# Performance work log

Hardware: AMD Instinct MI355X
Metric: run time of the kernel (lower is better)

The kernel has to match this reference:

```python
import jax, jax.numpy as jnp
import numpy as np

B, S, HID = 4, 2048, 1024
H, D = 16, 64  # num_attention_heads, attention_head_size


def setup_inputs() -> dict:
    key = jax.random.key(0)
    k1, k2, k3, k4 = jax.random.split(key, 4)
    scale = 0.02
    return {
        "hidden_states": jax.random.normal(k1, (B, S, HID), dtype=jnp.float32),
        "attention_mask": jnp.zeros((B, 1, 1, S), dtype=jnp.float32),
        "Wq": jax.random.normal(k2, (HID, HID), dtype=jnp.float32) * scale,
        "bq": jnp.zeros((HID,), dtype=jnp.float32),
        "Wk": jax.random.normal(k3, (HID, HID), dtype=jnp.float32) * scale,
        "bk": jnp.zeros((HID,), dtype=jnp.float32),
        "Wv": jax.random.normal(k4, (HID, HID), dtype=jnp.float32) * scale,
        "bv": jnp.zeros((HID,), dtype=jnp.float32),
    }


def _split_heads(x):
    # [B,S,HID] -> [B,H,S,D]
    b, s, _ = x.shape
    return x.reshape(b, s, H, D).transpose(0, 2, 1, 3)


def reference(hidden_states, attention_mask, Wq, bq, Wk, bk, Wv, bv):
    # nn.Linear applies x @ W.T + b
    q = _split_heads(hidden_states @ Wq.T + bq)  # [B,H,S,D]
    k = _split_heads(hidden_states @ Wk.T + bk)
    v = _split_heads(hidden_states @ Wv.T + bv)
    scores = jnp.einsum("bhqd,bhkd->bhqk", q, k) / jnp.sqrt(jnp.float32(D))
    scores = scores + attention_mask  # additive mask, broadcast [B,1,1,S]
    probs = jax.nn.softmax(scores, axis=-1)  # dropout prob = 0 -> identity
    ctx = jnp.einsum("bhqk,bhkd->bhqd", probs, v)  # [B,H,S,D]
    ctx = ctx.transpose(0, 2, 1, 3).reshape(hidden_states.shape[0], hidden_states.shape[1], HID)
    return ctx
```

## Files before the change

### kernel.cpp

```cpp
#include <hip/hip_runtime.h>
#include <stdint.h>

#define BB 4
#define SS 2048
#define HID 1024
#define NH 16
#define DH 64

using bf16x8 = __attribute__((ext_vector_type(8))) short;
using f32x4  = __attribute__((ext_vector_type(4))) float;

#define LOG2E 1.44269504088896340736f

__device__ __forceinline__ ushort f2bf(float f) {
  union { float f; uint32_t u; } v; v.f = f;
  return (ushort)((v.u + 0x7FFFu + ((v.u >> 16) & 1u)) >> 16);
}

__device__ __forceinline__ uint32_t cvt_pk_bf16(float a, float b) {
  uint32_t r;
  asm("v_cvt_pk_bf16_f32 %0, %1, %2" : "=v"(r) : "v"(a), "v"(b));
  return r;
}

__device__ __forceinline__ float exp2_hw(float x) {
  float r;
  asm("v_exp_f32 %0, %1" : "=v"(r) : "v"(x));
  return r;
}

__device__ __forceinline__ void gload_lds16(const ushort* g, ushort* l) {
  __builtin_amdgcn_global_load_lds(
      (const __attribute__((address_space(1))) uint32_t*)g,
      (__attribute__((address_space(3))) uint32_t*)l, 16, 0, 0);
}

__device__ __forceinline__ int vperm(int j) {
  return (j & 0x23) | ((j & 0x0C) << 1) | ((j & 0x10) >> 2);
}

__global__ void cvt_kernel(const float* __restrict__ x, const float* __restrict__ wq,
                           const float* __restrict__ wk, const float* __restrict__ wv,
                           const float* __restrict__ am,
                           ushort* __restrict__ xbf, ushort* __restrict__ wbf,
                           float* __restrict__ maskL) {
  const int64_t NX4 = (int64_t)BB * SS * HID / 4;
  const int64_t NW4 = (int64_t)HID * HID / 4;
  const int64_t NWT = 3 * NW4;
  int64_t i = (int64_t)blockIdx.x * blockDim.x + threadIdx.x;
  if (i >= NX4 + NWT) {
    const int64_t jm = i - (NX4 + NWT);
    float4 v = ((const float4*)am)[jm];
    v.x *= LOG2E; v.y *= LOG2E; v.z *= LOG2E; v.w *= LOG2E;
    ((float4*)maskL)[jm] = v;
    return;
  }
  float4 v;
  ushort4* dst;
  if (i < NX4) {
    v = ((const float4*)x)[i];
    dst = (ushort4*)xbf + i;
  } else {
    int64_t j = i - NX4;
    int w = (int)(j >> 18);
    int64_t k = j & (NW4 - 1);
    const float* src = (w == 0) ? wq : (w == 1) ? wk : wv;
    v = ((const float4*)src)[k];
    dst = (ushort4*)wbf + j;
  }
  ushort4 o;
  o.x = f2bf(v.x); o.y = f2bf(v.y); o.z = f2bf(v.z); o.w = f2bf(v.w);
  *dst = o;
}

__global__ __launch_bounds__(256) void qkv_gemm(
    const ushort* __restrict__ xbf, const ushort* __restrict__ wbf,
    const float* __restrict__ bq, const float* __restrict__ bk,
    const float* __restrict__ bv,
    ushort* __restrict__ qws, ushort* __restrict__ kws, ushort* __restrict__ vtws) {
  __shared__ short Al[2][128][32];
  __shared__ short Bl[2][128][32];
  const int tid = threadIdx.x, wid = tid >> 6, lane = tid & 63;
  const int m0 = blockIdx.x * 128, n0 = blockIdx.y * 128;
  const int wr = wid >> 1, wc = wid & 1;

  f32x4 acc[4][4];
#pragma unroll
  for (int i = 0; i < 4; ++i)
#pragma unroll
    for (int j = 0; j < 4; ++j)
#pragma unroll
      for (int r = 0; r < 4; ++r) acc[i][j][r] = 0.f;

  const int srow = wid * 32 + (lane >> 2);
  const int scol = (lane & 3) * 8;
  const ushort* ga = xbf + (int64_t)(m0 + srow) * HID + scol;
  const ushort* gb = wbf + (int64_t)(n0 + srow) * HID + scol;

  auto stage = [&](int bufsel, int kb) {
    const ushort* a = ga + kb * 32;
    const ushort* b = gb + kb * 32;
    gload_lds16(a,            (ushort*)&Al[bufsel][wid * 32][0]);
    gload_lds16(a + 16 * HID, (ushort*)&Al[bufsel][wid * 32 + 16][0]);
    gload_lds16(b,            (ushort*)&Bl[bufsel][wid * 32][0]);
    gload_lds16(b + 16 * HID, (ushort*)&Bl[bufsel][wid * 32 + 16][0]);
  };

  stage(0, 0);
  __syncthreads();
  const int colL = lane & 15, rowg = lane >> 4;
  for (int kb = 0; kb < HID / 32; ++kb) {
    const int buf = kb & 1;
    if (kb + 1 < HID / 32) stage(buf ^ 1, kb + 1);
    bf16x8 af[4], bfr[4];
#pragma unroll
    for (int i = 0; i < 4; ++i)
      af[i] = *(const bf16x8*)&Al[buf][wr * 64 + i * 16 + colL][rowg * 8];
#pragma unroll
    for (int j = 0; j < 4; ++j)
      bfr[j] = *(const bf16x8*)&Bl[buf][wc * 64 + j * 16 + colL][rowg * 8];
#pragma unroll
    for (int i = 0; i < 4; ++i)
#pragma unroll
      for (int j = 0; j < 4; ++j)
        acc[i][j] = __builtin_amdgcn_mfma_f32_16x16x32_bf16(af[i], bfr[j], acc[i][j], 0, 0, 0);
    __syncthreads();
  }

#pragma unroll
  for (int j = 0; j < 4; ++j) {
    const int n = n0 + wc * 64 + j * 16 + colL;
    const int which = n >> 10;
    const int c = n & 1023;
    const int h = c >> 6, d = c & 63;
    const float bias = ((which == 0) ? bq : (which == 1) ? bk : bv)[c];
#pragma unroll
    for (int i = 0; i < 4; ++i) {
      const int mb = m0 + wr * 64 + i * 16 + rowg * 4;
      const int b = mb >> 11, s = mb & 2047;
      const int bh = b * NH + h;
      if (which == 2) {
        ushort4 o;
        o.x = f2bf(acc[i][j][0] + bias);
        o.y = f2bf(acc[i][j][1] + bias);
        o.z = f2bf(acc[i][j][2] + bias);
        o.w = f2bf(acc[i][j][3] + bias);
        const int scol2 = (s & ~63) | vperm(s & 63);
        *(ushort4*)&vtws[((int64_t)bh * DH + d) * SS + scol2] = o;
      } else {
        ushort* dst = (which == 0) ? qws : kws;
#pragma unroll
        for (int r = 0; r < 4; ++r)
          dst[((int64_t)bh * SS + s + r) * DH + d] = f2bf(acc[i][j][r] + bias);
      }
    }
  }
}

__global__ __launch_bounds__(256, 4) void attn_kernel(
    const ushort* __restrict__ qws, const ushort* __restrict__ kws,
    const ushort* __restrict__ vtws, const float* __restrict__ maskL,
    float* __restrict__ out) {
  __shared__ short Kl[2][64][64];
  __shared__ short Vl[2][64][64];

  const int tid = threadIdx.x, wid = tid >> 6, lane = tid & 63;
  const int bh = blockIdx.x, qb = blockIdx.y;
  const int b = bh >> 4, h = bh & 15;
  const int64_t qkb = (int64_t)bh * SS * DH;
  const int64_t vb  = (int64_t)bh * DH * SS;
  const int q0 = qb * 128;
  const int colL = lane & 15, rowg = lane >> 4;
  const float SCL = 0.125f * LOG2E;

  const int srow = wid * 16 + (lane >> 3);
  const int swzc = (((lane & 7) * 16) ^ ((lane >> 3) << 4)) >> 1;
  const ushort* gk = kws + qkb + (int64_t)srow * DH + swzc;
  const ushort* gv = vtws + vb + (int64_t)srow * SS + swzc;
  ushort* ldsK = (ushort*)&Kl[0][0][0] + wid * 1024;
  ushort* ldsV = (ushort*)&Vl[0][0][0] + wid * 1024;

  auto stageKV = [&](int bufsel, int tt) {
    const ushort* k0 = gk + tt * 4096;
    gload_lds16(k0,       ldsK + bufsel * 4096);
    gload_lds16(k0 + 512, ldsK + bufsel * 4096 + 512);
    const ushort* v0 = gv + tt * 64;
    gload_lds16(v0,          ldsV + bufsel * 4096);
    gload_lds16(v0 + 8 * SS, ldsV + bufsel * 4096 + 512);
  };

  const int xsw = (colL & 7) << 4;
  const char* kb0 = (const char*)&Kl[0][0][0] + colL * 128 + ((rowg * 16) ^ xsw);
  const char* kb1 = (const char*)&Kl[0][0][0] + colL * 128 + ((64 + rowg * 16) ^ xsw);
  const char* vb0 = (const char*)&Vl[0][0][0] + colL * 128 + ((rowg * 16) ^ xsw);
  const char* vb1 = (const char*)&Vl[0][0][0] + colL * 128 + ((64 + rowg * 16) ^ xsw);

  bf16x8 qf[2][2];
#pragma unroll
  for (int qh = 0; qh < 2; ++qh) {
    const ushort* gq = qws + qkb + (int64_t)(q0 + wid * 32 + qh * 16 + colL) * DH + rowg * 8;
    qf[qh][0] = *(const bf16x8*)(gq);
    qf[qh][1] = *(const bf16x8*)(gq + 32);
  }

  const f32x4 FZERO = {0.f, 0.f, 0.f, 0.f};
  union OU { uint32_t u[4]; bf16x8 v; } onesu;
  onesu.u[0] = 0x3F803F80u; onesu.u[1] = 0x3F803F80u;
  onesu.u[2] = 0x3F803F80u; onesu.u[3] = 0x3F803F80u;
  const bf16x8 ONES = onesu.v;

  f32x4 accO[2][4];
  f32x4 accL[2];
#pragma unroll
  for (int qh = 0; qh < 2; ++qh) {
    accL[qh] = FZERO;
#pragma unroll
    for (int dt = 0; dt < 4; ++dt)
#pragma unroll
      for (int r = 0; r < 4; ++r) accO[qh][dt][r] = 0.f;
  }

  const float* mrow = maskL + b * SS + rowg * 4;

  stageKV(0, 0);
  __syncthreads();

  auto step = [&](int t, int bufc) {
    if (t + 1 < SS / 64) stageKV(bufc ^ 1, t + 1);

    f32x4 sc[2][4];
    __builtin_amdgcn_s_setprio(1);
#pragma unroll
    for (int kt = 0; kt < 4; ++kt) {
      bf16x8 kf0 = *(const bf16x8*)(kb0 + bufc * 8192 + kt * 2048);
      bf16x8 kf1 = *(const bf16x8*)(kb1 + bufc * 8192 + kt * 2048);
      sc[0][kt] = __builtin_amdgcn_mfma_f32_16x16x32_bf16(kf0, qf[0][0], FZERO, 0, 0, 0);
      sc[0][kt] = __builtin_amdgcn_mfma_f32_16x16x32_bf16(kf1, qf[0][1], sc[0][kt], 0, 0, 0);
      sc[1][kt] = __builtin_amdgcn_mfma_f32_16x16x32_bf16(kf0, qf[1][0], FZERO, 0, 0, 0);
      sc[1][kt] = __builtin_amdgcn_mfma_f32_16x16x32_bf16(kf1, qf[1][1], sc[1][kt], 0, 0, 0);
    }
    __builtin_amdgcn_s_setprio(0);

    float4 m4[4];
#pragma unroll
    for (int kt = 0; kt < 4; ++kt)
      m4[kt] = *(const float4*)(mrow + t * 64 + kt * 16);

    bf16x8 paf[2][2];
#pragma unroll
    for (int qh = 0; qh < 2; ++qh) {
#pragma unroll
      for (int kt = 0; kt < 4; ++kt) {
        sc[qh][kt][0] = exp2_hw(fmaf(sc[qh][kt][0], SCL, m4[kt].x));
        sc[qh][kt][1] = exp2_hw(fmaf(sc[qh][kt][1], SCL, m4[kt].y));
        sc[qh][kt][2] = exp2_hw(fmaf(sc[qh][kt][2], SCL, m4[kt].z));
        sc[qh][kt][3] = exp2_hw(fmaf(sc[qh][kt][3], SCL, m4[kt].w));
      }
      union PU { uint32_t u[4]; bf16x8 v; } p0, p1;
      p0.u[0] = cvt_pk_bf16(sc[qh][0][0], sc[qh][0][1]);
      p0.u[1] = cvt_pk_bf16(sc[qh][0][2], sc[qh][0][3]);
      p0.u[2] = cvt_pk_bf16(sc[qh][1][0], sc[qh][1][1]);
      p0.u[3] = cvt_pk_bf16(sc[qh][1][2], sc[qh][1][3]);
      p1.u[0] = cvt_pk_bf16(sc[qh][2][0], sc[qh][2][1]);
      p1.u[1] = cvt_pk_bf16(sc[qh][2][2], sc[qh][2][3]);
      p1.u[2] = cvt_pk_bf16(sc[qh][3][0], sc[qh][3][1]);
      p1.u[3] = cvt_pk_bf16(sc[qh][3][2], sc[qh][3][3]);
      paf[qh][0] = p0.v;
      paf[qh][1] = p1.v;
    }

    __builtin_amdgcn_s_setprio(1);
#pragma unroll
    for (int ks = 0; ks < 2; ++ks) {
      accL[0] = __builtin_amdgcn_mfma_f32_16x16x32_bf16(paf[0][ks], ONES, accL[0], 0, 0, 0);
      accL[1] = __builtin_amdgcn_mfma_f32_16x16x32_bf16(paf[1][ks], ONES, accL[1], 0, 0, 0);
#pragma unroll
      for (int dt = 0; dt < 4; ++dt) {
        bf16x8 vf = *(const bf16x8*)((ks == 0 ? vb0 : vb1) + bufc * 8192 + dt * 2048);
        accO[0][dt] = __builtin_amdgcn_mfma_f32_16x16x32_bf16(paf[0][ks], vf, accO[0][dt], 0, 0, 0);
        accO[1][dt] = __builtin_amdgcn_mfma_f32_16x16x32_bf16(paf[1][ks], vf, accO[1][dt], 0, 0, 0);
      }
    }
    __builtin_amdgcn_s_setprio(0);
    __syncthreads();
  };

  for (int t = 0; t < SS / 64; t += 2) {
    step(t, 0);
    step(t + 1, 1);
  }

#pragma unroll
  for (int qh = 0; qh < 2; ++qh) {
    float inv[4];
#pragma unroll
    for (int r = 0; r < 4; ++r) inv[r] = 1.0f / accL[qh][r];
#pragma unroll
    for (int dt = 0; dt < 4; ++dt)
#pragma unroll
      for (int r = 0; r < 4; ++r) {
        const int s = q0 + wid * 32 + qh * 16 + rowg * 4 + r;
        out[((int64_t)b * SS + s) * HID + h * DH + dt * 16 + colL] = accO[qh][dt][r] * inv[r];
      }
  }
}

extern "C" void kernel_launch(void* const* d_in, const int* in_sizes, int n_in,
                              void* d_out, int out_size, void* d_ws, size_t ws_size,
                              hipStream_t stream) {
  const float* x  = (const float*)d_in[0];
  const float* am = (const float*)d_in[1];
  const float* wq = (const float*)d_in[2];
  const float* bq = (const float*)d_in[3];
  const float* wk = (const float*)d_in[4];
  const float* bk = (const float*)d_in[5];
  const float* wv = (const float*)d_in[6];
  const float* bv = (const float*)d_in[7];
  float* out = (float*)d_out;
  char* ws = (char*)d_ws;

  ushort* xbf  = (ushort*)(ws);
  ushort* wbf  = (ushort*)(ws + 16777216);
  ushort* qws  = (ushort*)(ws + 23068672);
  ushort* kws  = (ushort*)(ws + 39845888);
  ushort* vtws = (ushort*)(ws + 56623104);
  float*  mskL = (float*)(ws + 73400320);

  hipLaunchKernelGGL(cvt_kernel, dim3(11272), dim3(256), 0, stream,
                     x, wq, wk, wv, am, xbf, wbf, mskL);
  hipLaunchKernelGGL(qkv_gemm, dim3(64, 24), dim3(256), 0, stream,
                     xbf, wbf, bq, bk, bv, qws, kws, vtws);
  hipLaunchKernelGGL(attn_kernel, dim3(64, 16), dim3(256), 0, stream,
                     qws, kws, vtws, mskL, out);
}
```

Before: 168.2 us.

## Rewrite QKV GEMM with 256x256 tiles, swizzled LDS, and phased prefetch pipeline

```diff
diff --git a/kernel.cpp b/kernel.cpp
--- a/kernel.cpp
+++ b/kernel.cpp
@@ -73,85 +73,130 @@
   *dst = o;
 }
 
-__global__ __launch_bounds__(256) void qkv_gemm(
+__global__ __launch_bounds__(512, 2) void qkv_gemm(
     const ushort* __restrict__ xbf, const ushort* __restrict__ wbf,
     const float* __restrict__ bq, const float* __restrict__ bk,
     const float* __restrict__ bv,
     ushort* __restrict__ qws, ushort* __restrict__ kws, ushort* __restrict__ vtws) {
-  __shared__ short Al[2][128][32];
-  __shared__ short Bl[2][128][32];
+  __shared__ short Al[2][256][64];
+  __shared__ short Bl[2][256][64];
+
   const int tid = threadIdx.x, wid = tid >> 6, lane = tid & 63;
-  const int m0 = blockIdx.x * 128, n0 = blockIdx.y * 128;
-  const int wr = wid >> 1, wc = wid & 1;
-
-  f32x4 acc[4][4];
-#pragma unroll
-  for (int i = 0; i < 4; ++i)
+  const int colL = lane & 15, rowg = lane >> 4;
+  const int wr = wid >> 2, wc = wid & 3;
+
+  const int wgid = (blockIdx.x & 7) * 48 + (blockIdx.x >> 3);
+  const int m0 = (wgid / 12) * 256;
+  const int n0 = (wgid % 12) * 256;
+
+  const int swzcol = (((tid & 7) * 16) ^ (((tid >> 3) & 7) << 4)) >> 1;
+  const ushort* aSrc = xbf + (int64_t)(m0 + (tid >> 3)) * HID + swzcol;
+  const ushort* bSrc = wbf + (int64_t)(n0 + (tid >> 3)) * HID + swzcol;
+  ushort* Al_u = (ushort*)&Al[0][0][0];
+  ushort* Bl_u = (ushort*)&Bl[0][0][0];
+
+  auto stageA = [&](int kt, int r, int ps) {
+    gload_lds16(aSrc + r * 64 * HID + kt * 64, Al_u + ps * 16384 + r * 4096 + wid * 512);
+  };
+  auto stageB = [&](int kt, int r, int ps) {
+    gload_lds16(bSrc + r * 64 * HID + kt * 64, Bl_u + ps * 16384 + r * 4096 + wid * 512);
+  };
+
+  const int xsw = (colL & 7) << 4;
+  const int offk0 = (rowg * 16) ^ xsw;
+  const int offk1 = (64 + rowg * 16) ^ xsw;
+  const int arow = (wr * 128 + colL) * 128;
+  const int brow = (wc * 64 + colL) * 128;
+  const char* AlC = (const char*)&Al[0][0][0];
+  const char* BlC = (const char*)&Bl[0][0][0];
+
+  f32x4 acc[8][4];
+#pragma unroll
+  for (int i = 0; i < 8; ++i)
 #pragma unroll
     for (int j = 0; j < 4; ++j)
 #pragma unroll
       for (int r = 0; r < 4; ++r) acc[i][j][r] = 0.f;
 
-  const int srow = wid * 32 + (lane >> 2);
-  const int scol = (lane & 3) * 8;
-  const ushort* ga = xbf + (int64_t)(m0 + srow) * HID + scol;
-  const ushort* gb = wbf + (int64_t)(n0 + srow) * HID + scol;
-
-  auto stage = [&](int bufsel, int kb) {
-    const ushort* a = ga + kb * 32;
-    const ushort* b = gb + kb * 32;
-    gload_lds16(a,            (ushort*)&Al[bufsel][wid * 32][0]);
-    gload_lds16(a + 16 * HID, (ushort*)&Al[bufsel][wid * 32 + 16][0]);
-    gload_lds16(b,            (ushort*)&Bl[bufsel][wid * 32][0]);
-    gload_lds16(b + 16 * HID, (ushort*)&Bl[bufsel][wid * 32 + 16][0]);
-  };
-
-  stage(0, 0);
-  __syncthreads();
-  const int colL = lane & 15, rowg = lane >> 4;
-  for (int kb = 0; kb < HID / 32; ++kb) {
-    const int buf = kb & 1;
-    if (kb + 1 < HID / 32) stage(buf ^ 1, kb + 1);
-    bf16x8 af[4], bfr[4];
-#pragma unroll
-    for (int i = 0; i < 4; ++i)
-      af[i] = *(const bf16x8*)&Al[buf][wr * 64 + i * 16 + colL][rowg * 8];
-#pragma unroll
-    for (int j = 0; j < 4; ++j)
-      bfr[j] = *(const bf16x8*)&Bl[buf][wc * 64 + j * 16 + colL][rowg * 8];
-#pragma unroll
-    for (int i = 0; i < 4; ++i)
-#pragma unroll
-      for (int j = 0; j < 4; ++j)
-        acc[i][j] = __builtin_amdgcn_mfma_f32_16x16x32_bf16(af[i], bfr[j], acc[i][j], 0, 0, 0);
-    __syncthreads();
-  }
-
-#pragma unroll
-  for (int j = 0; j < 4; ++j) {
-    const int n = n0 + wc * 64 + j * 16 + colL;
+  stageB(0, 0, 0); stageB(0, 1, 0); stageB(0, 2, 0); stageB(0, 3, 0);
+  stageA(0, 0, 0); stageA(0, 2, 0); stageA(0, 1, 0); stageA(0, 3, 0);
+  asm volatile("s_waitcnt vmcnt(2)" ::: "memory");
+  __builtin_amdgcn_s_barrier();
+
+#define DO_PHASE(P, S1, S2, PRE_BAR2)                                          \
+  {                                                                            \
+    const int mfa = 2 * (P), mfb = 2 * (P) + 1;                                \
+    bf16x8 aA0 = *(const bf16x8*)(kA0 + mfa * 2048);                           \
+    bf16x8 aA1 = *(const bf16x8*)(kA1 + mfa * 2048);                           \
+    bf16x8 aB0 = *(const bf16x8*)(kA0 + mfb * 2048);                           \
+    bf16x8 aB1 = *(const bf16x8*)(kA1 + mfb * 2048);                           \
+    S1; S2;                                                                    \
+    __builtin_amdgcn_s_barrier();                                              \
+    __builtin_amdgcn_s_setprio(1);                                             \
+    _Pragma("unroll")                                                          \
+    for (int nf = 0; nf < 4; ++nf) {                                           \
+      acc[mfa][nf] = __builtin_amdgcn_mfma_f32_16x16x32_bf16(aA0, bfr[nf][0], acc[mfa][nf], 0, 0, 0); \
+      acc[mfa][nf] = __builtin_amdgcn_mfma_f32_16x16x32_bf16(aA1, bfr[nf][1], acc[mfa][nf], 0, 0, 0); \
+      acc[mfb][nf] = __builtin_amdgcn_mfma_f32_16x16x32_bf16(aB0, bfr[nf][0], acc[mfb][nf], 0, 0, 0); \
+      acc[mfb][nf] = __builtin_amdgcn_mfma_f32_16x16x32_bf16(aB1, bfr[nf][1], acc[mfb][nf], 0, 0, 0); \
+    }                                                                          \
+    __builtin_amdgcn_s_setprio(0);                                             \
+    PRE_BAR2;                                                                  \
+    __builtin_amdgcn_s_barrier();                                              \
+  }
+
+  for (int t = 0; t < 16; ++t) {
+    const int p = t & 1;
+    const int ps = p ^ 1;
+    const bool st = (t < 15);
+    const int kt = t + 1;
+    const char* kA0 = AlC + p * 32768 + arow + offk0;
+    const char* kA1 = AlC + p * 32768 + arow + offk1;
+    const char* kB0 = BlC + p * 32768 + brow + offk0;
+    const char* kB1 = BlC + p * 32768 + brow + offk1;
+
+    bf16x8 bfr[4][2];
+#pragma unroll
+    for (int nf = 0; nf < 4; ++nf) {
+      bfr[nf][0] = *(const bf16x8*)(kB0 + nf * 2048);
+      bfr[nf][1] = *(const bf16x8*)(kB1 + nf * 2048);
+    }
+
+    DO_PHASE(0, if (st) stageB(kt, 0, ps), if (st) stageB(kt, 1, ps), )
+    DO_PHASE(1, if (st) stageB(kt, 2, ps), if (st) stageB(kt, 3, ps),
+             asm volatile("s_waitcnt vmcnt(4)" ::: "memory"))
+    DO_PHASE(2, if (st) stageA(kt, 0, ps), if (st) stageA(kt, 2, ps), )
+    DO_PHASE(3, if (st) stageA(kt, 1, ps), if (st) stageA(kt, 3, ps),
+             if (t == 14) { asm volatile("s_waitcnt vmcnt(0)" ::: "memory"); }
+             else        { asm volatile("s_waitcnt vmcnt(2)" ::: "memory"); })
+  }
+#undef DO_PHASE
+
+#pragma unroll
+  for (int nf = 0; nf < 4; ++nf) {
+    const int n = n0 + wc * 64 + nf * 16 + colL;
     const int which = n >> 10;
     const int c = n & 1023;
     const int h = c >> 6, d = c & 63;
     const float bias = ((which == 0) ? bq : (which == 1) ? bk : bv)[c];
 #pragma unroll
-    for (int i = 0; i < 4; ++i) {
-      const int mb = m0 + wr * 64 + i * 16 + rowg * 4;
+    for (int mf = 0; mf < 8; ++mf) {
+      const int mb = m0 + wr * 128 + mf * 16 + rowg * 4;
       const int b = mb >> 11, s = mb & 2047;
       const int bh = b * NH + h;
       if (which == 2) {
         ushort4 o;
-        o.x = f2bf(acc[i][j][0] + bias);
-        o.y = f2bf(acc[i][j][1] + bias);
-        o.z = f2bf(acc[i][j][2] + bias);
-        o.w = f2bf(acc[i][j][3] + bias);
+        o.x = f2bf(acc[mf][nf][0] + bias);
+        o.y = f2bf(acc[mf][nf][1] + bias);
+        o.z = f2bf(acc[mf][nf][2] + bias);
+        o.w = f2bf(acc[mf][nf][3] + bias);
         const int scol2 = (s & ~63) | vperm(s & 63);
         *(ushort4*)&vtws[((int64_t)bh * DH + d) * SS + scol2] = o;
       } else {
         ushort* dst = (which == 0) ? qws : kws;
 #pragma unroll
         for (int r = 0; r < 4; ++r)
-          dst[((int64_t)bh * SS + s + r) * DH + d] = f2bf(acc[i][j][r] + bias);
+          dst[((int64_t)bh * SS + s + r) * DH + d] = f2bf(acc[mf][nf][r] + bias);
       }
     }
   }
@@ -328,7 +373,7 @@
 
   hipLaunchKernelGGL(cvt_kernel, dim3(11272), dim3(256), 0, stream,
                      x, wq, wk, wv, am, xbf, wbf, mskL);
-  hipLaunchKernelGGL(qkv_gemm, dim3(64, 24), dim3(256), 0, stream,
+  hipLaunchKernelGGL(qkv_gemm, dim3(384), dim3(512), 0, stream,
                      xbf, wbf, bq, bk, bv, qws, kws, vtws);
   hipLaunchKernelGGL(attn_kernel, dim3(64, 16), dim3(256), 0, stream,
                      qws, kws, vtws, mskL, out);
```

Result: faster. 162.8 us (-3.3%).
